# Kernel tuning notes

Measured on AMD Instinct MI355X. Metric: run time of the kernel, lower is better.

Reference implementation:

```python
import jax, jax.numpy as jnp
import numpy as np

B, H, S, D = 4, 16, 2048, 128
D_MODEL = 128  # scale factor per module init


def setup_inputs() -> dict:
    key = jax.random.key(0)
    kq, kk, kv = jax.random.split(key, 3)
    Q = jax.random.normal(kq, (B, H, S, D), dtype=jnp.float32)
    K = jax.random.normal(kk, (B, H, S, D), dtype=jnp.float32)
    V = jax.random.normal(kv, (B, H, S, D), dtype=jnp.float32)
    return {"Q": Q, "K": K, "V": V}


def reference(Q, K, V):
    # scores: [B, H, S, S]
    scores = jnp.einsum("bhqd,bhkd->bhqk", Q, K) / np.sqrt(D_MODEL).astype(np.float32)
    # causal mask: lower-triangular keeps, upper becomes -inf
    q_idx = jnp.arange(S)[:, None]
    k_idx = jnp.arange(S)[None, :]
    causal = q_idx >= k_idx  # [S, S]
    scores = jnp.where(causal, scores, -jnp.inf)
    attn = jax.nn.softmax(scores, axis=-1)
    return jnp.einsum("bhqk,bhkd->bhqd", attn, V)
```

## Files before the change

kernel.cpp:

```cpp
#include <hip/hip_runtime.h>

typedef _Float16 f16;
typedef _Float16 f16x8 __attribute__((ext_vector_type(8)));
typedef float    f32x16 __attribute__((ext_vector_type(16)));
typedef int      i32x4 __attribute__((ext_vector_type(4)));

#define B_ 4
#define H_ 16
#define S_ 2048
#define D_ 128
#define KVB 32
#define KSTR 136
#define VTSTR 40

union U4 { i32x4 i; f16x8 h; };

__device__ __forceinline__ unsigned pk2(float a, float b) {
    auto v = __builtin_amdgcn_cvt_pkrtz(a, b);
    return __builtin_bit_cast(unsigned, v);
}

__device__ __forceinline__ f16x8 cvt8(const float4 a, const float4 b) {
    f16x8 h;
    h[0] = (f16)a.x; h[1] = (f16)a.y; h[2] = (f16)a.z; h[3] = (f16)a.w;
    h[4] = (f16)b.x; h[5] = (f16)b.y; h[6] = (f16)b.z; h[7] = (f16)b.w;
    return h;
}

__global__ __launch_bounds__(256)
void prep(const float* __restrict__ K, const float* __restrict__ V,
          f16* __restrict__ Kh, f16* __restrict__ Vtt)
{
    const int bid = blockIdx.x;
    const int bh  = bid >> 5;
    const int kb  = bid & 31;
    const int k0  = kb * 64;
    const int tid = threadIdx.x;

    const float* Kb = K + ((size_t)bh * S_ + k0) * D_;
    const float* Vb = V + ((size_t)bh * S_ + k0) * D_;
    f16* Khb = Kh + ((size_t)bh * S_ + k0) * D_;
    f16* Vtb = Vtt + (size_t)bh * S_ * D_ + (size_t)kb * 2 * (D_ * 32);

    #pragma unroll
    for (int it = 0; it < 4; ++it) {
        const int idx = tid + it * 256;
        const int row = idx >> 4, c8 = idx & 15;
        const float4 a = *(const float4*)(Kb + row * D_ + c8 * 8);
        const float4 b = *(const float4*)(Kb + row * D_ + c8 * 8 + 4);
        *(f16x8*)(Khb + row * D_ + c8 * 8) = cvt8(a, b);
    }
    #pragma unroll
    for (int it = 0; it < 4; ++it) {
        const int idx = tid + it * 256;
        const int d  = idx & 127;
        const int k8 = idx >> 7;
        const float* vp = Vb + (size_t)(k8 * 8) * D_ + d;
        f16x8 vh;
        #pragma unroll
        for (int e = 0; e < 8; ++e) vh[e] = (f16)vp[(size_t)e * D_];
        *(f16x8*)(Vtb + (size_t)(k8 >> 2) * (D_ * 32) + d * 32 + (k8 & 3) * 8) = vh;
    }
}

__global__ __launch_bounds__(256, 2)
void fattn12(const float* __restrict__ Qg, const f16* __restrict__ Khg,
             const f16* __restrict__ Vttg, float* __restrict__ Og)
{
    __shared__ __align__(16) f16 Klds[2][KVB * KSTR];
    __shared__ __align__(16) f16 Vt[2][128 * VTSTR];

    const int id  = blockIdx.x;
    const int xcd = id & 7;
    const int r   = id >> 3;
    const int bh  = xcd + 8 * (r & 7);
    const int p   = r >> 3;

    const int tid  = threadIdx.x;
    const int lane = tid & 63;
    const int l31  = lane & 31;
    const int h    = lane >> 5;
    const int wv   = tid >> 6;

    const float* Qb  = Qg   + (size_t)bh * S_ * D_;
    const f16*   Khb = Khg  + (size_t)bh * S_ * D_;
    const f16*   Vtb = Vttg + (size_t)bh * S_ * D_;
    float*       Ob  = Og   + (size_t)bh * S_ * D_;

    const f16* kS = Khb + (tid >> 4) * D_ + (tid & 15) * 8;
    const f16* vS = Vtb + (size_t)tid * 8;
    const int  kDo = (tid >> 4) * KSTR + (tid & 15) * 8;
    const int  vDo = (tid >> 2) * VTSTR + (tid & 3) * 8;

    i32x4 kr[2], vr[2];
    auto issue = [&](int kt) {
        const f16* kp = kS + ((size_t)kt << 12);
        const f16* vp = vS + ((size_t)kt << 12);
        kr[0] = *(const i32x4*)kp;
        kr[1] = *(const i32x4*)(kp + 2048);
        vr[0] = *(const i32x4*)vp;
        vr[1] = *(const i32x4*)(vp + 2048);
    };
    auto writeLds = [&](int buf) {
        f16* kb = &Klds[buf][0];
        f16* vb = &Vt[buf][0];
        *(i32x4*)(kb + kDo)              = kr[0];
        *(i32x4*)(kb + kDo + 16 * KSTR)  = kr[1];
        *(i32x4*)(vb + vDo)              = vr[0];
        *(i32x4*)(vb + vDo + 64 * VTSTR) = vr[1];
    };
    f16x8 qf[8];
    auto qkt = [&](int buf) {
        f32x16 a;
        #pragma unroll
        for (int rr = 0; rr < 16; ++rr) a[rr] = 0.f;
        #pragma unroll
        for (int dc = 0; dc < 8; ++dc) {
            const f16x8 kf = *(const f16x8*)&Klds[buf][l31 * KSTR + dc * 16 + h * 8];
            a = __builtin_amdgcn_mfma_f32_32x32x16_f16(kf, qf[dc], a, 0, 0, 0);
        }
        return a;
    };

    const float qmul = 0.08838834764831845f * 1.4426950408889634f;

    #pragma unroll 1
    for (int ph = 0; ph < 2; ++ph) {
        const int qt  = ph ? 15 - p : p;
        const int qw0 = qt * 128 + wv * 32;
        const int qg  = qw0 + l31;
        const int nkt = 4 * qt + 4;
        const int lastt = 4 * qt + wv;

        issue(0);
        {
            const float* Qrow = Qb + (size_t)(qw0 + l31) * D_;
            #pragma unroll
            for (int dc = 0; dc < 8; ++dc) {
                const float4 a = *(const float4*)(Qrow + dc * 16 + h * 8);
                const float4 b = *(const float4*)(Qrow + dc * 16 + h * 8 + 4);
                f16x8 q;
                q[0] = (f16)(a.x * qmul); q[1] = (f16)(a.y * qmul);
                q[2] = (f16)(a.z * qmul); q[3] = (f16)(a.w * qmul);
                q[4] = (f16)(b.x * qmul); q[5] = (f16)(b.y * qmul);
                q[6] = (f16)(b.z * qmul); q[7] = (f16)(b.w * qmul);
                qf[dc] = q;
            }
        }

        f32x16 acc[4];
        #pragma unroll
        for (int dt = 0; dt < 4; ++dt)
            #pragma unroll
            for (int rr = 0; rr < 16; ++rr) acc[dt][rr] = 0.f;
        float m_i = -1e30f, l_i = 0.f;

        __syncthreads();
        writeLds(0);
        issue(1);
        __syncthreads();

        f32x16 sv = qkt(0);

        for (int kt = 0; kt < nkt; ++kt) {
            const int cur  = kt & 1;
            const bool more = (kt + 1 < nkt);

            if (more) {
                __syncthreads();
                writeLds(cur ^ 1);
                if (kt + 2 < nkt) issue(kt + 2);
                __syncthreads();
            }

            __builtin_amdgcn_s_setprio(1);
            f32x16 svn;
            if (more && kt + 1 <= lastt) svn = qkt(cur ^ 1);

            if (kt <= lastt) {
                const int k0 = kt * KVB;
                if (k0 + 31 > qw0) {
                    #pragma unroll
                    for (int rr = 0; rr < 16; ++rr) {
                        const int kg = k0 + (rr & 3) + 8 * (rr >> 2) + 4 * h;
                        if (kg > qg) sv[rr] = -1e30f;
                    }
                }
                const float m1 = fmaxf(fmaxf(sv[0], sv[1]), sv[2]);
                const float m2 = fmaxf(fmaxf(sv[3], sv[4]), sv[5]);
                const float m3 = fmaxf(fmaxf(sv[6], sv[7]), sv[8]);
                const float m4 = fmaxf(fmaxf(sv[9], sv[10]), sv[11]);
                const float m5 = fmaxf(fmaxf(sv[12], sv[13]), sv[14]);
                float mx = fmaxf(fmaxf(m1, m2), m3);
                mx = fmaxf(fmaxf(mx, m4), m5);
                mx = fmaxf(mx, sv[15]);
                mx = fmaxf(mx, __shfl_xor(mx, 32));
                if (!__all(mx - m_i <= 8.0f)) {
                    const float mn = fmaxf(m_i, mx);
                    const float al = exp2f(m_i - mn);
                    m_i = mn;
                    l_i *= al;
                    float arow[16];
                    #pragma unroll
                    for (int rr = 0; rr < 16; ++rr)
                        arow[rr] = __shfl(al, (rr & 3) + 8 * (rr >> 2) + 4 * h);
                    #pragma unroll
                    for (int dt = 0; dt < 4; ++dt)
                        #pragma unroll
                        for (int rr = 0; rr < 16; ++rr) acc[dt][rr] *= arow[rr];
                }
                #pragma unroll
                for (int rr = 0; rr < 16; ++rr) sv[rr] = exp2f(sv[rr] - m_i);
                float s8[8];
                #pragma unroll
                for (int rr = 0; rr < 8; ++rr) s8[rr] = sv[2 * rr] + sv[2 * rr + 1];
                #pragma unroll
                for (int rr = 0; rr < 4; ++rr) s8[rr] += s8[rr + 4];
                s8[0] += s8[2]; s8[1] += s8[3];
                float rs = s8[0] + s8[1];
                rs += __shfl_xor(rs, 32);
                l_i += rs;
                U4 pa[2];
                {
                    unsigned dwp[8];
                    #pragma unroll
                    for (int m = 0; m < 8; ++m) dwp[m] = pk2(sv[2 * m], sv[2 * m + 1]);
                    #pragma unroll
                    for (int hf = 0; hf < 2; ++hf) {
                        const unsigned a0 = dwp[hf * 4 + 0], a1 = dwp[hf * 4 + 1];
                        const unsigned b0 = dwp[hf * 4 + 2], b1 = dwp[hf * 4 + 3];
                        const unsigned sa0 = (unsigned)__shfl_xor((int)a0, 32);
                        const unsigned sa1 = (unsigned)__shfl_xor((int)a1, 32);
                        const unsigned sb0 = (unsigned)__shfl_xor((int)b0, 32);
                        const unsigned sb1 = (unsigned)__shfl_xor((int)b1, 32);
                        i32x4 d;
                        d[0] = h ? (int)sb0 : (int)a0;
                        d[1] = h ? (int)sb1 : (int)a1;
                        d[2] = h ? (int)b0  : (int)sa0;
                        d[3] = h ? (int)b1  : (int)sa1;
                        pa[hf].i = d;
                    }
                }
                #pragma unroll
                for (int dt = 0; dt < 4; ++dt) {
                    const f16* vrow = &Vt[cur][(dt * 32 + l31) * VTSTR + h * 8];
                    const f16x8 vb0 = *(const f16x8*)(vrow + 0);
                    const f16x8 vb1 = *(const f16x8*)(vrow + 16);
                    acc[dt] = __builtin_amdgcn_mfma_f32_32x32x16_f16(pa[0].h, vb0, acc[dt], 0, 0, 0);
                    acc[dt] = __builtin_amdgcn_mfma_f32_32x32x16_f16(pa[1].h, vb1, acc[dt], 0, 0, 0);
                }
            }
            __builtin_amdgcn_s_setprio(0);

            if (more) sv = svn;
        }

        float li[16];
        #pragma unroll
        for (int rr = 0; rr < 16; ++rr) {
            const float lv = __shfl(l_i, (rr & 3) + 8 * (rr >> 2) + 4 * h);
            li[rr] = 1.0f / lv;
        }
        #pragma unroll
        for (int dt = 0; dt < 4; ++dt)
            #pragma unroll
            for (int rr = 0; rr < 16; ++rr) {
                const int row = qw0 + (rr & 3) + 8 * (rr >> 2) + 4 * h;
                Ob[(size_t)row * D_ + dt * 32 + l31] = acc[dt][rr] * li[rr];
            }
    }
}

__global__ __launch_bounds__(256, 3)
void fattn5(const float* __restrict__ Qg, const float* __restrict__ Kg,
            const float* __restrict__ Vg, float* __restrict__ Og)
{
    __shared__ __align__(16) f16 Klds[2][KVB * KSTR];
    __shared__ __align__(16) f16 Vt[2][128 * VTSTR];
    const int id  = blockIdx.x;
    const int xcd = id & 7;
    const int w   = id >> 3;
    const int qt  = 15 - (w & 15);
    const int bh  = xcd + 8 * (w >> 4);
    const int tid  = threadIdx.x;
    const int lane = tid & 63;
    const int wv   = tid >> 6;
    const int l31  = lane & 31;
    const int h    = lane >> 5;
    const int qw0 = qt * 128 + wv * 32;
    const int qg  = qw0 + l31;
    const size_t base = (size_t)bh * S_ * D_;
    const float* Qb = Qg + base;
    const float* Kb = Kg + base;
    const float* Vb = Vg + base;
    float*       Ob = Og + base;
    const int nkt = 4 * qt + 4;
    float4 kr[4];
    float  vr[16];
    auto issue = [&](int kt) {
        const int k0n = kt * KVB;
        #pragma unroll
        for (int it = 0; it < 2; ++it) {
            const int idx  = tid + it * 256;
            const int krow = idx >> 4;
            const int c8   = idx & 15;
            const float* kp = Kb + (size_t)(k0n + krow) * D_ + c8 * 8;
            kr[it * 2]     = *(const float4*)kp;
            kr[it * 2 + 1] = *(const float4*)(kp + 4);
            const int d  = idx & 127;
            const int k8 = idx >> 7;
            const float* vp = Vb + (size_t)(k0n + k8 * 8) * D_ + d;
            #pragma unroll
            for (int e = 0; e < 8; ++e) vr[it * 8 + e] = vp[(size_t)e * D_];
        }
    };
    auto writeLds = [&](int buf) {
        #pragma unroll
        for (int it = 0; it < 2; ++it) {
            const int idx  = tid + it * 256;
            const int krow = idx >> 4;
            const int c8   = idx & 15;
            *(f16x8*)&Klds[buf][krow * KSTR + c8 * 8] = cvt8(kr[it * 2], kr[it * 2 + 1]);
            const int d  = idx & 127;
            const int k8 = idx >> 7;
            f16x8 vh;
            #pragma unroll
            for (int e = 0; e < 8; ++e) vh[e] = (f16)vr[it * 8 + e];
            *(f16x8*)&Vt[buf][d * VTSTR + k8 * 8] = vh;
        }
    };
    const float qmul = 0.08838834764831845f * 1.4426950408889634f;
    f16x8 qf[8];
    {
        const float* Qrow = Qb + (size_t)(qw0 + l31) * D_;
        #pragma unroll
        for (int dc = 0; dc < 8; ++dc) {
            const float4 a = *(const float4*)(Qrow + dc * 16 + h * 8);
            const float4 b = *(const float4*)(Qrow + dc * 16 + h * 8 + 4);
            f16x8 q;
            q[0] = (f16)(a.x * qmul); q[1] = (f16)(a.y * qmul);
            q[2] = (f16)(a.z * qmul); q[3] = (f16)(a.w * qmul);
            q[4] = (f16)(b.x * qmul); q[5] = (f16)(b.y * qmul);
            q[6] = (f16)(b.z * qmul); q[7] = (f16)(b.w * qmul);
            qf[dc] = q;
        }
    }
    f32x16 acc[4];
    #pragma unroll
    for (int dt = 0; dt < 4; ++dt)
        #pragma unroll
        for (int rr = 0; rr < 16; ++rr) acc[dt][rr] = 0.f;
    float m_i = -1e30f, l_i = 0.f;
    issue(0);
    writeLds(0);
    if (nkt > 1) issue(1);
    __syncthreads();
    for (int kt = 0; kt < nkt; ++kt) {
        const int k0  = kt * KVB;
        const int cur = kt & 1;
        if (k0 <= qw0 + 31) {
            f32x16 sv;
            #pragma unroll
            for (int rr = 0; rr < 16; ++rr) sv[rr] = 0.f;
            #pragma unroll
            for (int dc = 0; dc < 8; ++dc) {
                const f16x8 kf = *(const f16x8*)&Klds[cur][l31 * KSTR + dc * 16 + h * 8];
                sv = __builtin_amdgcn_mfma_f32_32x32x16_f16(kf, qf[dc], sv, 0, 0, 0);
            }
            if (k0 + 31 > qw0) {
                #pragma unroll
                for (int rr = 0; rr < 16; ++rr) {
                    const int kg = k0 + (rr & 3) + 8 * (rr >> 2) + 4 * h;
                    if (kg > qg) sv[rr] = -1e30f;
                }
            }
            float mx = sv[0];
            #pragma unroll
            for (int rr = 1; rr < 16; ++rr) mx = fmaxf(mx, sv[rr]);
            mx = fmaxf(mx, __shfl_xor(mx, 32));
            if (!__all(mx - m_i <= 8.0f)) {
                const float mn = fmaxf(m_i, mx);
                const float al = exp2f(m_i - mn);
                m_i = mn;
                l_i *= al;
                float arow[16];
                #pragma unroll
                for (int rr = 0; rr < 16; ++rr)
                    arow[rr] = __shfl(al, (rr & 3) + 8 * (rr >> 2) + 4 * h);
                #pragma unroll
                for (int dt = 0; dt < 4; ++dt)
                    #pragma unroll
                    for (int rr = 0; rr < 16; ++rr) acc[dt][rr] *= arow[rr];
            }
            float rs = 0.f;
            #pragma unroll
            for (int rr = 0; rr < 16; ++rr) {
                sv[rr] = exp2f(sv[rr] - m_i);
                rs += sv[rr];
            }
            rs += __shfl_xor(rs, 32);
            l_i += rs;
            U4 pa[2];
            {
                unsigned dwp[8];
                #pragma unroll
                for (int m = 0; m < 8; ++m) dwp[m] = pk2(sv[2 * m], sv[2 * m + 1]);
                #pragma unroll
                for (int hf = 0; hf < 2; ++hf) {
                    const unsigned a0 = dwp[hf * 4 + 0], a1 = dwp[hf * 4 + 1];
                    const unsigned b0 = dwp[hf * 4 + 2], b1 = dwp[hf * 4 + 3];
                    const unsigned sa0 = (unsigned)__shfl_xor((int)a0, 32);
                    const unsigned sa1 = (unsigned)__shfl_xor((int)a1, 32);
                    const unsigned sb0 = (unsigned)__shfl_xor((int)b0, 32);
                    const unsigned sb1 = (unsigned)__shfl_xor((int)b1, 32);
                    i32x4 d;
                    d[0] = h ? (int)sb0 : (int)a0;
                    d[1] = h ? (int)sb1 : (int)a1;
                    d[2] = h ? (int)b0  : (int)sa0;
                    d[3] = h ? (int)b1  : (int)sa1;
                    pa[hf].i = d;
                }
            }
            #pragma unroll
            for (int dt = 0; dt < 4; ++dt) {
                const f16* vrow = &Vt[cur][(dt * 32 + l31) * VTSTR + h * 8];
                const f16x8 vb0 = *(const f16x8*)(vrow + 0);
                const f16x8 vb1 = *(const f16x8*)(vrow + 16);
                acc[dt] = __builtin_amdgcn_mfma_f32_32x32x16_f16(pa[0].h, vb0, acc[dt], 0, 0, 0);
                acc[dt] = __builtin_amdgcn_mfma_f32_32x32x16_f16(pa[1].h, vb1, acc[dt], 0, 0, 0);
            }
        }
        if (kt + 1 < nkt) {
            writeLds(cur ^ 1);
            if (kt + 2 < nkt) issue(kt + 2);
            __syncthreads();
        }
    }
    float li[16];
    #pragma unroll
    for (int rr = 0; rr < 16; ++rr) {
        const float lv = __shfl(l_i, (rr & 3) + 8 * (rr >> 2) + 4 * h);
        li[rr] = 1.0f / lv;
    }
    #pragma unroll
    for (int dt = 0; dt < 4; ++dt)
        #pragma unroll
        for (int rr = 0; rr < 16; ++rr) {
            const int row = qw0 + (rr & 3) + 8 * (rr >> 2) + 4 * h;
            Ob[(size_t)row * D_ + dt * 32 + l31] = acc[dt][rr] * li[rr];
        }
}

extern "C" void kernel_launch(void* const* d_in, const int* in_sizes, int n_in,
                              void* d_out, int out_size, void* d_ws, size_t ws_size,
                              hipStream_t stream) {
    (void)in_sizes; (void)n_in; (void)out_size;
    const float* Q = (const float*)d_in[0];
    const float* K = (const float*)d_in[1];
    const float* V = (const float*)d_in[2];
    float* O = (float*)d_out;
    const size_t elems  = (size_t)B_ * H_ * S_ * D_;
    const size_t needKV = elems * 2 * sizeof(f16);
    if (ws_size >= needKV) {
        f16* Kh  = (f16*)d_ws;
        f16* Vtt = Kh + elems;
        prep<<<dim3(B_ * H_ * (S_ / 64)), dim3(256), 0, stream>>>(K, V, Kh, Vtt);
        fattn12<<<dim3(512), dim3(256), 0, stream>>>(Q, Kh, Vtt, O);
    } else {
        fattn5<<<dim3((S_ / 128) * B_ * H_), dim3(256), 0, stream>>>(Q, K, V, O);
    }
}
```

Baseline: 160.0 us.

## Triple-buffer K/V LDS with one barrier per step; permute V layout to drop shuffles

The attention kernel moves from double to triple buffering of K and V tiles in LDS, rotating buffer indices so each iteration needs one __syncthreads instead of two. The prep kernel now stores transposed V in a permuted k-order, which lets the P fragment be packed directly from the MFMA accumulator without the cross-half lane shuffles and selects. The cost is more LDS per block, which could limit occupancy at two blocks per CU, and a V layout tied to this kernel's fragment ordering.

```diff
diff --git a/kernel.cpp b/kernel.cpp
--- a/kernel.cpp
+++ b/kernel.cpp
@@ -1,6 +1,7 @@
 #include <hip/hip_runtime.h>
 
 typedef _Float16 f16;
+typedef _Float16 f16x4 __attribute__((ext_vector_type(4)));
 typedef _Float16 f16x8 __attribute__((ext_vector_type(8)));
 typedef float    f32x16 __attribute__((ext_vector_type(16)));
 typedef int      i32x4 __attribute__((ext_vector_type(4)));
@@ -56,19 +57,24 @@
         const int d  = idx & 127;
         const int k8 = idx >> 7;
         const float* vp = Vb + (size_t)(k8 * 8) * D_ + d;
-        f16x8 vh;
-        #pragma unroll
-        for (int e = 0; e < 8; ++e) vh[e] = (f16)vp[(size_t)e * D_];
-        *(f16x8*)(Vtb + (size_t)(k8 >> 2) * (D_ * 32) + d * 32 + (k8 & 3) * 8) = vh;
+        f16x4 lo, hi;
+        #pragma unroll
+        for (int e = 0; e < 4; ++e) lo[e] = (f16)vp[(size_t)e * D_];
+        #pragma unroll
+        for (int e = 0; e < 4; ++e) hi[e] = (f16)vp[(size_t)(e + 4) * D_];
+        f16* dst = Vtb + (size_t)(k8 >> 2) * (D_ * 32) + d * 32
+                 + ((k8 >> 1) & 1) * 16 + (k8 & 1) * 4;
+        *(f16x4*)(dst)     = lo;
+        *(f16x4*)(dst + 8) = hi;
     }
 }
 
 __global__ __launch_bounds__(256, 2)
-void fattn12(const float* __restrict__ Qg, const f16* __restrict__ Khg,
+void fattn13(const float* __restrict__ Qg, const f16* __restrict__ Khg,
              const f16* __restrict__ Vttg, float* __restrict__ Og)
 {
-    __shared__ __align__(16) f16 Klds[2][KVB * KSTR];
-    __shared__ __align__(16) f16 Vt[2][128 * VTSTR];
+    __shared__ __align__(16) f16 Klds[3][KVB * KSTR];
+    __shared__ __align__(16) f16 Vt[3][128 * VTSTR];
 
     const int id  = blockIdx.x;
     const int xcd = id & 7;
@@ -132,7 +138,6 @@
         const int nkt = 4 * qt + 4;
         const int lastt = 4 * qt + wv;
 
-        issue(0);
         {
             const float* Qrow = Qb + (size_t)(qw0 + l31) * D_;
             #pragma unroll
@@ -156,26 +161,23 @@
         float m_i = -1e30f, l_i = 0.f;
 
         __syncthreads();
-        writeLds(0);
-        issue(1);
+        issue(0);  writeLds(0);
+        issue(1);  writeLds(1);
+        if (nkt > 2) issue(2);
         __syncthreads();
-
         f32x16 sv = qkt(0);
 
+        int bB = 0, bA = 1, bW = 2;
         for (int kt = 0; kt < nkt; ++kt) {
-            const int cur  = kt & 1;
-            const bool more = (kt + 1 < nkt);
-
-            if (more) {
-                __syncthreads();
-                writeLds(cur ^ 1);
-                if (kt + 2 < nkt) issue(kt + 2);
-                __syncthreads();
+            __syncthreads();
+            if (kt + 2 < nkt) {
+                writeLds(bW);
+                if (kt + 3 < nkt) issue(kt + 3);
             }
 
             __builtin_amdgcn_s_setprio(1);
             f32x16 svn;
-            if (more && kt + 1 <= lastt) svn = qkt(cur ^ 1);
+            if (kt + 1 < nkt && kt + 1 <= lastt) svn = qkt(bA);
 
             if (kt <= lastt) {
                 const int k0 = kt * KVB;
@@ -221,29 +223,13 @@
                 rs += __shfl_xor(rs, 32);
                 l_i += rs;
                 U4 pa[2];
-                {
-                    unsigned dwp[8];
-                    #pragma unroll
-                    for (int m = 0; m < 8; ++m) dwp[m] = pk2(sv[2 * m], sv[2 * m + 1]);
-                    #pragma unroll
-                    for (int hf = 0; hf < 2; ++hf) {
-                        const unsigned a0 = dwp[hf * 4 + 0], a1 = dwp[hf * 4 + 1];
-                        const unsigned b0 = dwp[hf * 4 + 2], b1 = dwp[hf * 4 + 3];
-                        const unsigned sa0 = (unsigned)__shfl_xor((int)a0, 32);
-                        const unsigned sa1 = (unsigned)__shfl_xor((int)a1, 32);
-                        const unsigned sb0 = (unsigned)__shfl_xor((int)b0, 32);
-                        const unsigned sb1 = (unsigned)__shfl_xor((int)b1, 32);
-                        i32x4 d;
-                        d[0] = h ? (int)sb0 : (int)a0;
-                        d[1] = h ? (int)sb1 : (int)a1;
-                        d[2] = h ? (int)b0  : (int)sa0;
-                        d[3] = h ? (int)b1  : (int)sa1;
-                        pa[hf].i = d;
-                    }
-                }
+                #pragma unroll
+                for (int m = 0; m < 4; ++m) pa[0].i[m] = (int)pk2(sv[2 * m],     sv[2 * m + 1]);
+                #pragma unroll
+                for (int m = 0; m < 4; ++m) pa[1].i[m] = (int)pk2(sv[8 + 2 * m], sv[9 + 2 * m]);
                 #pragma unroll
                 for (int dt = 0; dt < 4; ++dt) {
-                    const f16* vrow = &Vt[cur][(dt * 32 + l31) * VTSTR + h * 8];
+                    const f16* vrow = &Vt[bB][(dt * 32 + l31) * VTSTR + h * 8];
                     const f16x8 vb0 = *(const f16x8*)(vrow + 0);
                     const f16x8 vb1 = *(const f16x8*)(vrow + 16);
                     acc[dt] = __builtin_amdgcn_mfma_f32_32x32x16_f16(pa[0].h, vb0, acc[dt], 0, 0, 0);
@@ -252,7 +238,8 @@
             }
             __builtin_amdgcn_s_setprio(0);
 
-            if (more) sv = svn;
+            if (kt + 1 < nkt) sv = svn;
+            const int t = bB; bB = bA; bA = bW; bW = t;
         }
 
         float li[16];
@@ -465,7 +452,7 @@
         f16* Kh  = (f16*)d_ws;
         f16* Vtt = Kh + elems;
         prep<<<dim3(B_ * H_ * (S_ / 64)), dim3(256), 0, stream>>>(K, V, Kh, Vtt);
-        fattn12<<<dim3(512), dim3(256), 0, stream>>>(Q, Kh, Vtt, O);
+        fattn13<<<dim3(512), dim3(256), 0, stream>>>(Q, Kh, Vtt, O);
     } else {
         fattn5<<<dim3((S_ / 128) * B_ * H_), dim3(256), 0, stream>>>(Q, K, V, O);
     }
```

Result: no change. 161.7 us (+1.1%).
